# Performance work log

Measured on AMD Instinct MI355X. Metric: run time of the kernel, lower is better.

Reference implementation:

```python
import jax, jax.numpy as jnp
import numpy as np

B, T, C, H = 8, 1024, 1024, 16
D = C // H  # head size 64
EPS = 1e-5

def layernorm(x, g, b):
    m = jnp.mean(x, axis=-1, keepdims=True)
    v = jnp.var(x, axis=-1, keepdims=True)
    return (x - m) * jax.lax.rsqrt(v + EPS) * g + b

def setup_inputs() -> dict:
    key = jax.random.key(0)
    ks = jax.random.split(key, 12)
    s = 1.0 / np.sqrt(C)
    return {
        "x": jax.random.normal(ks[0], (B, T, C), dtype=jnp.float32),
        "mask": jnp.ones((B, 1, 1, T), dtype=jnp.int32),
        "Wq": jax.random.normal(ks[1], (C, C), dtype=jnp.float32) * s,
        "Wk": jax.random.normal(ks[2], (C, C), dtype=jnp.float32) * s,
        "Wv": jax.random.normal(ks[3], (C, C), dtype=jnp.float32) * s,
        "Wo": jax.random.normal(ks[4], (C, C), dtype=jnp.float32) * s,
        "bo": jnp.zeros((C,), dtype=jnp.float32),
        "ln1_g": jnp.ones((C,), dtype=jnp.float32),
        "ln1_b": jnp.zeros((C,), dtype=jnp.float32),
        "ln3_g": jnp.ones((C,), dtype=jnp.float32),
        "ln3_b": jnp.zeros((C,), dtype=jnp.float32),
        "W1": jax.random.normal(ks[5], (C, 4 * C), dtype=jnp.float32) * s,
        "b1": jnp.zeros((4 * C,), dtype=jnp.float32),
        "W2": jax.random.normal(ks[6], (4 * C, C), dtype=jnp.float32) * (1.0 / np.sqrt(4 * C)),
        "b2": jnp.zeros((C,), dtype=jnp.float32),
    }

def reference(x, mask, Wq, Wk, Wv, Wo, bo, ln1_g, ln1_b, ln3_g, ln3_b, W1, b1, W2, b2):
    # --- self-attention sublayer (pre-LN, residual) ---
    xn = layernorm(x, ln1_g, ln1_b)                      # [B,T,C]
    q = (xn @ Wq).reshape(B, T, H, D)                    # [B,T,H,D]
    k = (xn @ Wk).reshape(B, T, H, D)
    v = (xn @ Wv).reshape(B, T, H, D)
    scores = jnp.einsum('bqhd,bkhd->bhqk', q, k) / np.sqrt(D)  # [B,H,T,T]
    scores = jnp.where(mask == 0, -jnp.inf, scores)      # padding mask [B,1,1,T] broadcasts
    attn = jax.nn.softmax(scores, axis=-1)               # dropout=0.0 -> identity
    o = jnp.einsum('bhqk,bkhd->bqhd', attn, v).reshape(B, T, C)
    x = x + o @ Wo + bo
    # --- feed-forward sublayer (pre-LN, residual) ---
    h = layernorm(x, ln3_g, ln3_b)
    ff = jax.nn.relu(h @ W1 + b1) @ W2 + b2
    return x + ff
```

## Files before the change

kernel.cpp:

```cpp
#include <hip/hip_runtime.h>
#include <stdint.h>

typedef unsigned short u16;
typedef __bf16 bf16x8 __attribute__((ext_vector_type(8)));
typedef float f32x4 __attribute__((ext_vector_type(4)));

#define B_ 8
#define T_ 1024
#define C_ 1024
#define H_ 16
#define D_ 64
#define M_TOT 8192
#define FF_ 4096

__device__ __forceinline__ u16 f2bf(float f) {
  union { float f; unsigned u; } c; c.f = f;
  unsigned u = c.u;
  return (u16)((u + 0x7FFFu + ((u >> 16) & 1u)) >> 16);
}

__device__ __forceinline__ void g2l16(const void* g, void* l) {
  __builtin_amdgcn_global_load_lds((const __attribute__((address_space(1))) void*)g,
                                   (__attribute__((address_space(3))) void*)l, 16, 0, 0);
}

__global__ __launch_bounds__(256) void trans_f32_bf16(const float* __restrict__ in,
                                                      u16* __restrict__ out, int R, int C) {
  __shared__ float t[32][33];
  int c0 = blockIdx.x * 32, r0 = blockIdx.y * 32;
  int tx = threadIdx.x & 31, ty = threadIdx.x >> 5;
#pragma unroll
  for (int i = ty; i < 32; i += 8)
    t[i][tx] = in[(size_t)(r0 + i) * C + c0 + tx];
  __syncthreads();
#pragma unroll
  for (int i = ty; i < 32; i += 8)
    out[(size_t)(c0 + i) * R + r0 + tx] = f2bf(t[tx][i]);
}

__global__ __launch_bounds__(256) void vtrans_bf16(const u16* __restrict__ v,
                                                   u16* __restrict__ vt) {
  __shared__ u16 t[64][66];
  int bh = blockIdx.y;
  int b = bh >> 4, h = bh & 15;
  int t0 = blockIdx.x * 64;
  int tx = threadIdx.x & 63, w = threadIdx.x >> 6;
#pragma unroll
  for (int i = w; i < 64; i += 4)
    t[i][tx] = v[(size_t)(b * T_ + t0 + i) * C_ + h * D_ + tx];
  __syncthreads();
#pragma unroll
  for (int d = w; d < 64; d += 4)
    vt[((size_t)bh * D_ + d) * T_ + t0 + tx] = t[tx][d];
}

__global__ __launch_bounds__(256) void ln_f32_bf16(const float* __restrict__ x,
                                                   const float* __restrict__ g,
                                                   const float* __restrict__ bt,
                                                   u16* __restrict__ out) {
  int row = blockIdx.x, tid = threadIdx.x;
  const float4* xr = (const float4*)(x + (size_t)row * C_);
  float4 a = xr[tid];
  float s = a.x + a.y + a.z + a.w;
  float ss = a.x * a.x + a.y * a.y + a.z * a.z + a.w * a.w;
#pragma unroll
  for (int m = 1; m < 64; m <<= 1) { s += __shfl_xor(s, m); ss += __shfl_xor(ss, m); }
  __shared__ float red[8];
  int wave = tid >> 6, lane = tid & 63;
  if (lane == 0) { red[wave] = s; red[wave + 4] = ss; }
  __syncthreads();
  s = red[0] + red[1] + red[2] + red[3];
  ss = red[4] + red[5] + red[6] + red[7];
  float mean = s * (1.0f / C_);
  float rstd = rsqrtf(ss * (1.0f / C_) - mean * mean + 1e-5f);
  float4 gg = ((const float4*)g)[tid];
  float4 bb = ((const float4*)bt)[tid];
  u16* op = out + (size_t)row * C_ + tid * 4;
  op[0] = f2bf((a.x - mean) * rstd * gg.x + bb.x);
  op[1] = f2bf((a.y - mean) * rstd * gg.y + bb.y);
  op[2] = f2bf((a.z - mean) * rstd * gg.z + bb.z);
  op[3] = f2bf((a.w - mean) * rstd * gg.w + bb.w);
}

template <int EPI>
__global__ __launch_bounds__(256) void gemm_bf16(const u16* __restrict__ A,
                                                 const u16* __restrict__ BT,
                                                 u16* __restrict__ outb, float* __restrict__ outf,
                                                 const float* __restrict__ bias,
                                                 const float* __restrict__ resid,
                                                 int M, int N, int K) {
  __shared__ u16 As[128 * 32];
  __shared__ u16 Bs[128 * 32];
  int tid = threadIdx.x, wave = tid >> 6, lane = tid & 63;
  int m0 = blockIdx.y * 128, n0 = blockIdx.x * 128;
  int wr = wave >> 1, wc = wave & 1;
  int frow = lane & 15, fk = (lane >> 4) * 8;
  f32x4 acc[4][4] = {};
  for (int k0 = 0; k0 < K; k0 += 32) {
    __syncthreads();
#pragma unroll
    for (int i = 0; i < 2; i++) {
      int c = i * 256 + tid;
      const u16* ga = A + (size_t)(m0 + (c >> 2)) * K + k0 + (c & 3) * 8;
      const u16* gb = BT + (size_t)(n0 + (c >> 2)) * K + k0 + (c & 3) * 8;
      g2l16(ga, As + (i * 256 + wave * 64) * 8);
      g2l16(gb, Bs + (i * 256 + wave * 64) * 8);
    }
    asm volatile("s_waitcnt vmcnt(0)" ::: "memory");
    __syncthreads();
    bf16x8 af[4], bfr[4];
#pragma unroll
    for (int m = 0; m < 4; m++) af[m] = *(const bf16x8*)(As + (wr * 64 + m * 16 + frow) * 32 + fk);
#pragma unroll
    for (int n = 0; n < 4; n++) bfr[n] = *(const bf16x8*)(Bs + (wc * 64 + n * 16 + frow) * 32 + fk);
#pragma unroll
    for (int m = 0; m < 4; m++)
#pragma unroll
      for (int n = 0; n < 4; n++)
        acc[m][n] = __builtin_amdgcn_mfma_f32_16x16x32_bf16(af[m], bfr[n], acc[m][n], 0, 0, 0);
  }
#pragma unroll
  for (int m = 0; m < 4; m++)
#pragma unroll
    for (int n = 0; n < 4; n++)
#pragma unroll
      for (int r = 0; r < 4; r++) {
        int row = m0 + wr * 64 + m * 16 + (lane >> 4) * 4 + r;
        int col = n0 + wc * 64 + n * 16 + (lane & 15);
        float v = acc[m][n][r];
        if (EPI == 0) {
          outb[(size_t)row * N + col] = f2bf(v);
        } else if (EPI == 1) {
          v += bias[col];
          v = fmaxf(v, 0.f);
          outb[(size_t)row * N + col] = f2bf(v);
        } else {
          v += bias[col] + resid[(size_t)row * N + col];
          outf[(size_t)row * N + col] = v;
        }
      }
}

__global__ __launch_bounds__(256) void attn_kernel(const u16* __restrict__ q,
                                                   const u16* __restrict__ k,
                                                   const u16* __restrict__ vt,
                                                   const int* __restrict__ mask,
                                                   u16* __restrict__ o) {
  int tid = threadIdx.x, wave = tid >> 6, lane = tid & 63;
  int qt = blockIdx.x;
  int bh = blockIdx.y;
  int b = bh >> 4, h = bh & 15;
  const size_t base = ((size_t)b * T_) * C_ + h * D_;
  int l15 = lane & 15, g = lane >> 4;

  int qrow = qt * 64 + wave * 16 + l15;
  int dk = g * 8;
  bf16x8 qf0 = *(const bf16x8*)(q + base + (size_t)qrow * C_ + dk);
  bf16x8 qf1 = *(const bf16x8*)(q + base + (size_t)qrow * C_ + dk + 32);

  const u16* vbase = vt + (size_t)bh * D_ * T_;

  f32x4 oacc[4] = {};
  float mrun[4], lrun[4];
#pragma unroll
  for (int r = 0; r < 4; r++) { mrun[r] = -1e30f; lrun[r] = 0.f; }

  __shared__ u16 plds[4][16 * 72];
  u16* pw = plds[wave];
  const int wsw = g * 8;
  const int rsw = ((l15 >> 2) & 3) * 8;

  for (int kt = 0; kt < T_ / 64; ++kt) {
    f32x4 s[4];
#pragma unroll
    for (int c = 0; c < 4; c++) {
      int kcol = kt * 64 + c * 16 + l15;
      const u16* kp = k + base + (size_t)kcol * C_;
      bf16x8 k0 = *(const bf16x8*)(kp + dk);
      bf16x8 k1 = *(const bf16x8*)(kp + dk + 32);
      f32x4 a = {};
      a = __builtin_amdgcn_mfma_f32_16x16x32_bf16(qf0, k0, a, 0, 0, 0);
      a = __builtin_amdgcn_mfma_f32_16x16x32_bf16(qf1, k1, a, 0, 0, 0);
      int mv = mask[b * T_ + kcol];
#pragma unroll
      for (int r = 0; r < 4; r++) a[r] = mv ? a[r] * 0.125f : -1e30f;
      s[c] = a;
    }
    float tmax[4];
#pragma unroll
    for (int r = 0; r < 4; r++)
      tmax[r] = fmaxf(fmaxf(s[0][r], s[1][r]), fmaxf(s[2][r], s[3][r]));
#pragma unroll
    for (int m = 1; m < 16; m <<= 1)
#pragma unroll
      for (int r = 0; r < 4; r++) tmax[r] = fmaxf(tmax[r], __shfl_xor(tmax[r], m));
    float alpha[4];
#pragma unroll
    for (int r = 0; r < 4; r++) {
      float nm = fmaxf(mrun[r], tmax[r]);
      alpha[r] = __expf(mrun[r] - nm);
      mrun[r] = nm;
    }
    float psum[4] = {0.f, 0.f, 0.f, 0.f};
#pragma unroll
    for (int c = 0; c < 4; c++)
#pragma unroll
      for (int r = 0; r < 4; r++) {
        float p = __expf(s[c][r] - mrun[r]);
        s[c][r] = p;
        psum[r] += p;
      }
#pragma unroll
    for (int m = 1; m < 16; m <<= 1)
#pragma unroll
      for (int r = 0; r < 4; r++) psum[r] += __shfl_xor(psum[r], m);
#pragma unroll
    for (int r = 0; r < 4; r++) lrun[r] = lrun[r] * alpha[r] + psum[r];
#pragma unroll
    for (int n = 0; n < 4; n++)
#pragma unroll
      for (int r = 0; r < 4; r++) oacc[n][r] *= alpha[r];
#pragma unroll
    for (int c = 0; c < 4; c++)
#pragma unroll
      for (int r = 0; r < 4; r++)
        pw[(4 * g + r) * 72 + ((c * 16 + l15) ^ wsw)] = f2bf(s[c][r]);
    bf16x8 pa0 = *(const bf16x8*)(pw + l15 * 72 + (0 * 32 + (g * 8 ^ rsw)));
    bf16x8 pa1 = *(const bf16x8*)(pw + l15 * 72 + (1 * 32 + (g * 8 ^ rsw)));
#pragma unroll
    for (int n = 0; n < 4; n++) {
      const u16* vp = vbase + (size_t)(n * 16 + l15) * T_ + kt * 64 + g * 8;
      bf16x8 v0 = *(const bf16x8*)(vp);
      bf16x8 v1 = *(const bf16x8*)(vp + 32);
      oacc[n] = __builtin_amdgcn_mfma_f32_16x16x32_bf16(pa0, v0, oacc[n], 0, 0, 0);
      oacc[n] = __builtin_amdgcn_mfma_f32_16x16x32_bf16(pa1, v1, oacc[n], 0, 0, 0);
    }
  }
#pragma unroll
  for (int n = 0; n < 4; n++)
#pragma unroll
    for (int r = 0; r < 4; r++) {
      int row = qt * 64 + wave * 16 + g * 4 + r;
      o[((size_t)b * T_ + row) * C_ + h * D_ + n * 16 + l15] =
          f2bf(oacc[n][r] / lrun[r]);
    }
}

extern "C" void kernel_launch(void* const* d_in, const int* in_sizes, int n_in,
                              void* d_out, int out_size, void* d_ws, size_t ws_size,
                              hipStream_t stream) {
  const float* x    = (const float*)d_in[0];
  const int*   mask = (const int*)d_in[1];
  const float* Wq   = (const float*)d_in[2];
  const float* Wk   = (const float*)d_in[3];
  const float* Wv   = (const float*)d_in[4];
  const float* Wo   = (const float*)d_in[5];
  const float* bo   = (const float*)d_in[6];
  const float* ln1g = (const float*)d_in[7];
  const float* ln1b = (const float*)d_in[8];
  const float* ln3g = (const float*)d_in[9];
  const float* ln3b = (const float*)d_in[10];
  const float* W1   = (const float*)d_in[11];
  const float* b1   = (const float*)d_in[12];
  const float* W2   = (const float*)d_in[13];
  const float* b2   = (const float*)d_in[14];
  float* out = (float*)d_out;

  char* ws = (char*)d_ws;
  const size_t MB = 1024 * 1024;
  u16* WqT = (u16*)(ws + 0 * MB);
  u16* WkT = (u16*)(ws + 2 * MB);
  u16* WvT = (u16*)(ws + 4 * MB);
  u16* WoT = (u16*)(ws + 6 * MB);
  u16* W1T = (u16*)(ws + 8 * MB);
  u16* W2T = (u16*)(ws + 16 * MB);
  u16* xn  = (u16*)(ws + 24 * MB);
  u16* qb  = (u16*)(ws + 40 * MB);
  u16* kb  = (u16*)(ws + 56 * MB);
  u16* vb  = (u16*)(ws + 72 * MB);
  u16* ob  = (u16*)(ws + 88 * MB);
  float* x2 = (float*)(ws + 104 * MB);
  u16* vT  = xn;
  u16* hb  = xn;
  u16* ff1 = qb;

  dim3 blk(256);
  trans_f32_bf16<<<dim3(32, 32), blk, 0, stream>>>(Wq, WqT, 1024, 1024);
  trans_f32_bf16<<<dim3(32, 32), blk, 0, stream>>>(Wk, WkT, 1024, 1024);
  trans_f32_bf16<<<dim3(32, 32), blk, 0, stream>>>(Wv, WvT, 1024, 1024);
  trans_f32_bf16<<<dim3(32, 32), blk, 0, stream>>>(Wo, WoT, 1024, 1024);
  trans_f32_bf16<<<dim3(128, 32), blk, 0, stream>>>(W1, W1T, 1024, 4096);
  trans_f32_bf16<<<dim3(32, 128), blk, 0, stream>>>(W2, W2T, 4096, 1024);
  ln_f32_bf16<<<8192, blk, 0, stream>>>(x, ln1g, ln1b, xn);
  gemm_bf16<0><<<dim3(8, 64), blk, 0, stream>>>(xn, WqT, qb, nullptr, nullptr, nullptr, 8192, 1024, 1024);
  gemm_bf16<0><<<dim3(8, 64), blk, 0, stream>>>(xn, WkT, kb, nullptr, nullptr, nullptr, 8192, 1024, 1024);
  gemm_bf16<0><<<dim3(8, 64), blk, 0, stream>>>(xn, WvT, vb, nullptr, nullptr, nullptr, 8192, 1024, 1024);
  vtrans_bf16<<<dim3(16, 128), blk, 0, stream>>>(vb, vT);
  attn_kernel<<<dim3(16, 128), blk, 0, stream>>>(qb, kb, vT, mask, ob);
  gemm_bf16<2><<<dim3(8, 64), blk, 0, stream>>>(ob, WoT, nullptr, x2, bo, x, 8192, 1024, 1024);
  ln_f32_bf16<<<8192, blk, 0, stream>>>(x2, ln3g, ln3b, hb);
  gemm_bf16<1><<<dim3(32, 64), blk, 0, stream>>>(hb, W1T, ff1, nullptr, b1, nullptr, 8192, 4096, 1024);
  gemm_bf16<2><<<dim3(8, 64), blk, 0, stream>>>(ff1, W2T, nullptr, out, b2, x2, 8192, 1024, 4096);
}
```

Baseline: 749.3 us.

## Stage K/V tiles in LDS with double-buffered async global-to-LDS loads

Each attention block previously had all four waves load the same K and V tiles straight from global memory. Now the block cooperatively stages each 64x64 K and V tile into swizzled LDS, using double-buffered global_load_lds so the next tile is fetched while the current one is computed. This is meant to remove redundant global traffic and hide load latency, at the cost of extra LDS use (about 34KB) and a block barrier per iteration. Mask loads are also hoisted ahead of the MFMAs.

New measurement: 632.8 us. 1.18x faster.

```diff
diff --git a/kernel.cpp b/kernel.cpp
--- a/kernel.cpp
+++ b/kernel.cpp
@@ -146,6 +146,10 @@
                                                    const u16* __restrict__ vt,
                                                    const int* __restrict__ mask,
                                                    u16* __restrict__ o) {
+  __shared__ __attribute__((aligned(16))) u16 kbuf[2][64 * 64];
+  __shared__ __attribute__((aligned(16))) u16 vbuf[2][64 * 64];
+  __shared__ __attribute__((aligned(16))) u16 plds[4][16 * 72];
+
   int tid = threadIdx.x, wave = tid >> 6, lane = tid & 63;
   int qt = blockIdx.x;
   int bh = blockIdx.y;
@@ -158,32 +162,64 @@
   bf16x8 qf0 = *(const bf16x8*)(q + base + (size_t)qrow * C_ + dk);
   bf16x8 qf1 = *(const bf16x8*)(q + base + (size_t)qrow * C_ + dk + 32);
 
-  const u16* vbase = vt + (size_t)bh * D_ * T_;
+  const u16* vtb = vt + (size_t)bh * D_ * T_;
+
+  int c0 = tid, r0s = c0 >> 3, cc0 = c0 & 7, sc0 = cc0 ^ (r0s & 7);
+  int c1 = 256 + tid, r1s = c1 >> 3, cc1 = c1 & 7, sc1 = cc1 ^ (r1s & 7);
+  const u16* ksrc0 = k + base + (size_t)r0s * C_ + sc0 * 8;
+  const u16* ksrc1 = k + base + (size_t)r1s * C_ + sc1 * 8;
+  const u16* vsrc0 = vtb + (size_t)r0s * T_ + sc0 * 8;
+  const u16* vsrc1 = vtb + (size_t)r1s * T_ + sc1 * 8;
+  int dst0 = (0 * 256 + wave * 64) * 8;
+  int dst1 = (1 * 256 + wave * 64) * 8;
 
   f32x4 oacc[4] = {};
   float mrun[4], lrun[4];
 #pragma unroll
   for (int r = 0; r < 4; r++) { mrun[r] = -1e30f; lrun[r] = 0.f; }
 
-  __shared__ u16 plds[4][16 * 72];
   u16* pw = plds[wave];
   const int wsw = g * 8;
   const int rsw = ((l15 >> 2) & 3) * 8;
+  const int swz0 = (g ^ (l15 & 7)) * 8;
+  const int swz1 = ((g + 4) ^ (l15 & 7)) * 8;
+
+  {
+    g2l16(ksrc0, kbuf[0] + dst0);
+    g2l16(ksrc1, kbuf[0] + dst1);
+    g2l16(vsrc0, vbuf[0] + dst0);
+    g2l16(vsrc1, vbuf[0] + dst1);
+  }
+  asm volatile("s_waitcnt vmcnt(0)" ::: "memory");
+  __syncthreads();
 
   for (int kt = 0; kt < T_ / 64; ++kt) {
+    int cur = kt & 1;
+    if (kt < T_ / 64 - 1) {
+      int nxt = cur ^ 1;
+      size_t ko = (size_t)(kt + 1) * 64 * C_;
+      size_t vo = (size_t)(kt + 1) * 64;
+      g2l16(ksrc0 + ko, kbuf[nxt] + dst0);
+      g2l16(ksrc1 + ko, kbuf[nxt] + dst1);
+      g2l16(vsrc0 + vo, vbuf[nxt] + dst0);
+      g2l16(vsrc1 + vo, vbuf[nxt] + dst1);
+    }
+    int mv[4];
+#pragma unroll
+    for (int c = 0; c < 4; c++) mv[c] = mask[b * T_ + kt * 64 + c * 16 + l15];
+
+    const u16* kb = kbuf[cur];
     f32x4 s[4];
 #pragma unroll
     for (int c = 0; c < 4; c++) {
-      int kcol = kt * 64 + c * 16 + l15;
-      const u16* kp = k + base + (size_t)kcol * C_;
-      bf16x8 k0 = *(const bf16x8*)(kp + dk);
-      bf16x8 k1 = *(const bf16x8*)(kp + dk + 32);
+      const u16* kp = kb + (c * 16 + l15) * 64;
+      bf16x8 k0 = *(const bf16x8*)(kp + swz0);
+      bf16x8 k1 = *(const bf16x8*)(kp + swz1);
       f32x4 a = {};
       a = __builtin_amdgcn_mfma_f32_16x16x32_bf16(qf0, k0, a, 0, 0, 0);
       a = __builtin_amdgcn_mfma_f32_16x16x32_bf16(qf1, k1, a, 0, 0, 0);
-      int mv = mask[b * T_ + kcol];
-#pragma unroll
-      for (int r = 0; r < 4; r++) a[r] = mv ? a[r] * 0.125f : -1e30f;
+#pragma unroll
+      for (int r = 0; r < 4; r++) a[r] = mv[c] ? a[r] * 0.125f : -1e30f;
       s[c] = a;
     }
     float tmax[4];
@@ -227,14 +263,17 @@
         pw[(4 * g + r) * 72 + ((c * 16 + l15) ^ wsw)] = f2bf(s[c][r]);
     bf16x8 pa0 = *(const bf16x8*)(pw + l15 * 72 + (0 * 32 + (g * 8 ^ rsw)));
     bf16x8 pa1 = *(const bf16x8*)(pw + l15 * 72 + (1 * 32 + (g * 8 ^ rsw)));
+    const u16* vb2 = vbuf[cur];
 #pragma unroll
     for (int n = 0; n < 4; n++) {
-      const u16* vp = vbase + (size_t)(n * 16 + l15) * T_ + kt * 64 + g * 8;
-      bf16x8 v0 = *(const bf16x8*)(vp);
-      bf16x8 v1 = *(const bf16x8*)(vp + 32);
+      const u16* vp = vb2 + (n * 16 + l15) * 64;
+      bf16x8 v0 = *(const bf16x8*)(vp + swz0);
+      bf16x8 v1 = *(const bf16x8*)(vp + swz1);
       oacc[n] = __builtin_amdgcn_mfma_f32_16x16x32_bf16(pa0, v0, oacc[n], 0, 0, 0);
       oacc[n] = __builtin_amdgcn_mfma_f32_16x16x32_bf16(pa1, v1, oacc[n], 0, 0, 0);
     }
+    asm volatile("s_waitcnt vmcnt(0)" ::: "memory");
+    __syncthreads();
   }
 #pragma unroll
   for (int n = 0; n < 4; n++)
```
